# Optimization experiments

Measured on AMD Instinct MI355X. Metric: run time of the kernel, lower is better.

## Reference

```python
import jax, jax.numpy as jnp
import numpy as np

SELF_OBS_DIM = 18
NEIGHBOR_OBS_DIM = 6
HIDDEN = 256
NUM_NEIGHBORS = 6
BATCH = 131072


def setup_inputs() -> dict:
    key = jax.random.key(0)
    k1, k2, k3, k4, k5, k6 = jax.random.split(key, 6)
    obs_dim = SELF_OBS_DIM + NEIGHBOR_OBS_DIM * NUM_NEIGHBORS
    self_obs = jax.random.normal(k1, (BATCH, SELF_OBS_DIM), dtype=jnp.float32)
    obs = jax.random.normal(k2, (BATCH, obs_dim), dtype=jnp.float32)
    # MLP params (PyTorch Linear default init scale ~ 1/sqrt(fan_in))
    W1 = jax.random.uniform(k3, (NEIGHBOR_OBS_DIM, HIDDEN), minval=-1.0, maxval=1.0) / np.sqrt(NEIGHBOR_OBS_DIM)
    b1 = jax.random.uniform(k4, (HIDDEN,), minval=-1.0, maxval=1.0) / np.sqrt(NEIGHBOR_OBS_DIM)
    W2 = jax.random.uniform(k5, (HIDDEN, HIDDEN), minval=-1.0, maxval=1.0) / np.sqrt(HIDDEN)
    b2 = jax.random.uniform(k6, (HIDDEN,), minval=-1.0, maxval=1.0) / np.sqrt(HIDDEN)
    return {
        "self_obs": self_obs,
        "obs": obs,
        "W1": W1.astype(jnp.float32),
        "b1": b1.astype(jnp.float32),
        "W2": W2.astype(jnp.float32),
        "b2": b2.astype(jnp.float32),
        "all_neighbor_obs_size": NEIGHBOR_OBS_DIM * NUM_NEIGHBORS,
        "batch_size": BATCH,
    }


def reference(self_obs, obs, W1, b1, W2, b2, all_neighbor_obs_size, batch_size):
    # slice out neighbor observations: obs[:, self_obs_dim : self_obs_dim + all_neighbor_obs_size]
    obs_neighbors = obs[:, SELF_OBS_DIM:SELF_OBS_DIM + all_neighbor_obs_size]
    # reshape to per-neighbor rows: [B * num_neighbors, neighbor_obs_dim]
    x = obs_neighbors.reshape(-1, NEIGHBOR_OBS_DIM)
    # shared 2-layer MLP with tanh (sample-factory default nonlinearity)
    h = jnp.tanh(x @ W1 + b1)
    h = jnp.tanh(h @ W2 + b2)
    # [B, num_neighbors, hidden] -> mean over neighbor axis
    neighbor_embeds = h.reshape(batch_size, -1, HIDDEN)
    mean_embed = jnp.mean(neighbor_embeds, axis=1)
    return mean_embed
```

## Files before the change

### kernel.cpp

```cpp
#include <hip/hip_runtime.h>


#define HID     256
#define OBSD    54
#define SELFD   18
#define TILE_B  8
#define TILE_R  48
#define LDA     264
#define BATCHN  131072
#define NTILES  (BATCHN / TILE_B)
#define GRID_WG 2048
#define TANH_K  2.8853900817779268f

typedef __attribute__((ext_vector_type(8))) short bf16x8;
typedef __attribute__((ext_vector_type(4))) float f32x4;

__device__ __forceinline__ unsigned cvt_pk_bf16(float lo, float hi) {
    unsigned r;
    asm("v_cvt_pk_bf16_f32 %0, %1, %2" : "=v"(r) : "v"(lo), "v"(hi));
    return r;
}

__device__ __forceinline__ float tanh_z(float z) {
    float t = __builtin_amdgcn_exp2f(z);
    return 1.0f - 2.0f * __builtin_amdgcn_rcpf(t + 1.0f);
}

__device__ __forceinline__ unsigned bfbits(float f) {
    unsigned u = __float_as_uint(f);
    u += 0x7fffu + ((u >> 16) & 1u);
    return u >> 16;
}

__global__ void prep(const float* __restrict__ W1, const float* __restrict__ W2,
                     short* __restrict__ w1t, short* __restrict__ w2t) {
    int idx = blockIdx.x * 256 + threadIdx.x;
    if (idx < 65536) {
        int n = idx >> 8, k = idx & 255;
        w2t[idx] = (short)bfbits(W2[k * HID + n] * TANH_K);
    } else {
        int j = idx - 65536;
        int n = j >> 5, k = j & 31;
        w1t[j] = (k < 6) ? (short)bfbits(W1[k * HID + n] * TANH_K) : (short)0;
    }
}

__global__ __launch_bounds__(512, 4) void qenc_main(
        const float* __restrict__ obs,
        const short* __restrict__ w1t,
        const float* __restrict__ b1,
        const short* __restrict__ w2t,
        const float* __restrict__ b2,
        float* __restrict__ out)
{
    __shared__ short a2[2][TILE_R * LDA];

    const int tid  = threadIdx.x;
    const int wave = tid >> 6;
    const int lane = tid & 63;
    const int q    = lane >> 4;
    const int c16  = lane & 15;
    const int colbase = wave * 32;

    bf16x8 Bf[8][2];
    #pragma unroll
    for (int kk = 0; kk < 8; ++kk)
        #pragma unroll
        for (int ct = 0; ct < 2; ++ct)
            Bf[kk][ct] = *(const bf16x8*)
                (w2t + (colbase + ct * 16 + c16) * HID + kk * 32 + q * 8);

    bf16x8 B1f[2];
    #pragma unroll
    for (int ct = 0; ct < 2; ++ct)
        B1f[ct] = *(const bf16x8*)(w1t + (colbase + ct * 16 + c16) * 32 + q * 8);

    float b1s[2][4];
    #pragma unroll
    for (int ct = 0; ct < 2; ++ct)
        #pragma unroll
        for (int g = 0; g < 4; ++g)
            b1s[ct][g] = b1[colbase + ct * 16 + q * 4 + g] * TANH_K;
    float b2s[2];
    #pragma unroll
    for (int ct = 0; ct < 2; ++ct)
        b2s[ct] = b2[colbase + ct * 16 + c16] * TANH_K;

    int soff[3];
    #pragma unroll
    for (int rt = 0; rt < 3; ++rt) {
        int row = rt * 16 + c16;
        soff[rt] = (row / 6) * OBSD + SELFD + (row % 6) * 6;
    }

    const int blA = 2 * q + (q & 1);
    const int blB = (q < 2) ? (q + 5) : (q - 1);
    const bool isq0 = (q == 0), isq1 = (q == 1), isq2 = (q == 2);

    int pb = 0;
    for (int tile = blockIdx.x; tile < NTILES; tile += GRID_WG) {
        const size_t obase = (size_t)tile * (TILE_B * OBSD);
        short* __restrict__ a = a2[pb];

        #pragma unroll
        for (int rt = 0; rt < 3; ++rt) {
            const float* src = obs + obase + soff[rt];
            float2 f0 = *(const float2*)(src);
            float2 f1 = *(const float2*)(src + 2);
            float2 f2 = *(const float2*)(src + 4);
            union { unsigned w[4]; bf16x8 v; } xf;
            xf.w[0] = cvt_pk_bf16(f0.x, f0.y);
            xf.w[1] = cvt_pk_bf16(f1.x, f1.y);
            xf.w[2] = cvt_pk_bf16(f2.x, f2.y);
            xf.w[3] = 0u;
            #pragma unroll
            for (int ct = 0; ct < 2; ++ct) {
                f32x4 c = __builtin_amdgcn_mfma_f32_16x16x32_bf16(
                    B1f[ct], xf.v,
                    (f32x4){b1s[ct][0], b1s[ct][1], b1s[ct][2], b1s[ct][3]},
                    0, 0, 0);
                float t0 = tanh_z(c[0]);
                float t1 = tanh_z(c[1]);
                float t2 = tanh_z(c[2]);
                float t3 = tanh_z(c[3]);
                uint2 dd;
                dd.x = cvt_pk_bf16(t0, t1);
                dd.y = cvt_pk_bf16(t2, t3);
                *(uint2*)&a[(rt * 16 + c16) * LDA + colbase + ct * 16 + q * 4] = dd;
            }
        }
        __syncthreads();

        f32x4 acc[3][2];
        #pragma unroll
        for (int rt = 0; rt < 3; ++rt)
            #pragma unroll
            for (int ct = 0; ct < 2; ++ct)
                acc[rt][ct] = (f32x4){b2s[ct], b2s[ct], b2s[ct], b2s[ct]};

        #pragma unroll
        for (int kk = 0; kk < 8; ++kk) {
            bf16x8 Af[3];
            #pragma unroll
            for (int rt = 0; rt < 3; ++rt)
                Af[rt] = *(const bf16x8*)&a[(rt * 16 + c16) * LDA + kk * 32 + q * 8];
            #pragma unroll
            for (int rt = 0; rt < 3; ++rt)
                #pragma unroll
                for (int ct = 0; ct < 2; ++ct)
                    acc[rt][ct] = __builtin_amdgcn_mfma_f32_16x16x32_bf16(
                        Af[rt], Bf[kk][ct], acc[rt][ct], 0, 0, 0);
        }

        const int b0 = tile * TILE_B;
        #pragma unroll
        for (int ct = 0; ct < 2; ++ct) {
            const int col = colbase + ct * 16 + c16;
            float s[3], uu[3], f[3];
            #pragma unroll
            for (int rt = 0; rt < 3; ++rt) {
                float t0 = tanh_z(acc[rt][ct][0]);
                float t1 = tanh_z(acc[rt][ct][1]);
                float t2 = tanh_z(acc[rt][ct][2]);
                float t3 = tanh_z(acc[rt][ct][3]);
                s[rt] = t0 + t1; uu[rt] = t2 + t3; f[rt] = s[rt] + uu[rt];
            }
            float A = isq1 ? s[0] : f[0];
            float B = isq1 ? uu[0] : (isq2 ? f[1] : s[1]);
            float C = isq2 ? s[2] : (isq1 ? f[1] : uu[1]);
            float D = isq2 ? uu[2] : f[2];
            float p1 = isq0 ? C : (isq1 ? A : (isq2 ? D : B));
            float p2 = (q < 2) ? B : C;
            float r1 = __shfl_xor(p1, 16);
            float r2 = __shfl_xor(p2, 48);
            float own1 = (isq0 ? A : (isq1 ? C : (isq2 ? B : D))) + r1;
            float own2 = ((q < 2) ? D : A) + r2;
            out[(size_t)(b0 + blA) * HID + col] = own1 * (1.0f / 6.0f);
            out[(size_t)(b0 + blB) * HID + col] = own2 * (1.0f / 6.0f);
        }
        pb ^= 1;
    }
}

extern "C" void kernel_launch(void* const* d_in, const int* in_sizes, int n_in,
                              void* d_out, int out_size, void* d_ws, size_t ws_size,
                              hipStream_t stream) {
    const float* obs = (const float*)d_in[1];
    const float* W1  = (const float*)d_in[2];
    const float* b1  = (const float*)d_in[3];
    const float* W2  = (const float*)d_in[4];
    const float* b2  = (const float*)d_in[5];
    float* outp = (float*)d_out;

    short* w2t = (short*)d_ws;
    short* w1t = (short*)((char*)d_ws + 131072);

    prep<<<288, 256, 0, stream>>>(W1, W2, w1t, w2t);
    qenc_main<<<GRID_WG, 512, 0, stream>>>(obs, w1t, b1, w2t, b2, outp);
}
```

Measured before the change: 341.6 us.

## Prefetch next tile's obs into registers and single-buffer LDS with explicit barriers

Result: slower. 350.6 us (+2.6%).

```diff
diff --git a/kernel.cpp b/kernel.cpp
--- a/kernel.cpp
+++ b/kernel.cpp
@@ -26,6 +26,13 @@
     return 1.0f - 2.0f * __builtin_amdgcn_rcpf(t + 1.0f);
 }
 
+__device__ __forceinline__ void lds_barrier() {
+    __builtin_amdgcn_sched_barrier(0);
+    asm volatile("s_waitcnt lgkmcnt(0)" ::: "memory");
+    __builtin_amdgcn_s_barrier();
+    __builtin_amdgcn_sched_barrier(0);
+}
+
 __device__ __forceinline__ unsigned bfbits(float f) {
     unsigned u = __float_as_uint(f);
     u += 0x7fffu + ((u >> 16) & 1u);
@@ -53,7 +60,7 @@
         const float* __restrict__ b2,
         float* __restrict__ out)
 {
-    __shared__ short a2[2][TILE_R * LDA];
+    __shared__ short a[TILE_R * LDA];
 
     const int tid  = threadIdx.x;
     const int wave = tid >> 6;
@@ -97,21 +104,26 @@
     const int blB = (q < 2) ? (q + 5) : (q - 1);
     const bool isq0 = (q == 0), isq1 = (q == 1), isq2 = (q == 2);
 
-    int pb = 0;
+    float2 pf0[3], pf1[3], pf2[3];
+    {
+        const float* pbase = obs + (size_t)blockIdx.x * (TILE_B * OBSD);
+        #pragma unroll
+        for (int rt = 0; rt < 3; ++rt) {
+            const float* src = pbase + soff[rt];
+            pf0[rt] = *(const float2*)(src);
+            pf1[rt] = *(const float2*)(src + 2);
+            pf2[rt] = *(const float2*)(src + 4);
+        }
+    }
+
     for (int tile = blockIdx.x; tile < NTILES; tile += GRID_WG) {
-        const size_t obase = (size_t)tile * (TILE_B * OBSD);
-        short* __restrict__ a = a2[pb];
 
         #pragma unroll
         for (int rt = 0; rt < 3; ++rt) {
-            const float* src = obs + obase + soff[rt];
-            float2 f0 = *(const float2*)(src);
-            float2 f1 = *(const float2*)(src + 2);
-            float2 f2 = *(const float2*)(src + 4);
             union { unsigned w[4]; bf16x8 v; } xf;
-            xf.w[0] = cvt_pk_bf16(f0.x, f0.y);
-            xf.w[1] = cvt_pk_bf16(f1.x, f1.y);
-            xf.w[2] = cvt_pk_bf16(f2.x, f2.y);
+            xf.w[0] = cvt_pk_bf16(pf0[rt].x, pf0[rt].y);
+            xf.w[1] = cvt_pk_bf16(pf1[rt].x, pf1[rt].y);
+            xf.w[2] = cvt_pk_bf16(pf2[rt].x, pf2[rt].y);
             xf.w[3] = 0u;
             #pragma unroll
             for (int ct = 0; ct < 2; ++ct) {
@@ -129,7 +141,20 @@
                 *(uint2*)&a[(rt * 16 + c16) * LDA + colbase + ct * 16 + q * 4] = dd;
             }
         }
-        __syncthreads();
+        lds_barrier();
+
+        {
+            int ptile = tile + GRID_WG;
+            if (ptile >= NTILES) ptile = tile;
+            const float* pbase = obs + (size_t)ptile * (TILE_B * OBSD);
+            #pragma unroll
+            for (int rt = 0; rt < 3; ++rt) {
+                const float* src = pbase + soff[rt];
+                pf0[rt] = *(const float2*)(src);
+                pf1[rt] = *(const float2*)(src + 2);
+                pf2[rt] = *(const float2*)(src + 4);
+            }
+        }
 
         f32x4 acc[3][2];
         #pragma unroll
@@ -178,7 +203,7 @@
             out[(size_t)(b0 + blA) * HID + col] = own1 * (1.0f / 6.0f);
             out[(size_t)(b0 + blB) * HID + col] = own2 * (1.0f / 6.0f);
         }
-        pb ^= 1;
+        lds_barrier();
     }
 }
 
```
